# Kernel tuning notes

Measured on AMD Instinct MI355X. Metric: run time of the kernel, lower is better.

The kernel has to match this reference:

```python
import jax, jax.numpy as jnp
import numpy as np

BS, SEQ, ENC, DEC, HEADS, INTERM = 32, 2048, 512, 512, 8, 128
IH = INTERM * HEADS


def setup_inputs() -> dict:
    key = jax.random.key(0)
    ks = jax.random.split(key, 16)
    s = 0.02
    return {
        "enc": jax.random.normal(ks[0], (BS, SEQ, ENC), jnp.float32),
        "dec": jax.random.normal(ks[1], (BS, 1, DEC + ENC), jnp.float32),
        "kappa": jax.random.uniform(ks[2], (BS, 1, HEADS), jnp.float32),
        "mask": jnp.ones((BS, SEQ, 1), jnp.float32),
        "Wv": jax.random.normal(ks[3], (ENC, IH), jnp.float32) * s,
        "bv": jnp.zeros((IH,), jnp.float32),
        "Wq": jax.random.normal(ks[4], (DEC + ENC, IH), jnp.float32) * s,
        "bq": jnp.zeros((IH,), jnp.float32),
        "Wf": jax.random.normal(ks[5], (IH, HEADS), jnp.float32) * s,
        "bf": jnp.zeros((HEADS,), jnp.float32),
        "Wb": jax.random.normal(ks[6], (DEC + ENC, HEADS), jnp.float32) * s,
        "bb": jnp.zeros((HEADS,), jnp.float32),
        "Wk": jax.random.normal(ks[7], (DEC + ENC, HEADS), jnp.float32) * s,
        "bk": jnp.zeros((HEADS,), jnp.float32),
        "Wfc": jax.random.normal(ks[8], (ENC * HEADS, ENC), jnp.float32) * s,
        "bfc": jnp.zeros((ENC,), jnp.float32),
    }


def reference(enc, dec, kappa, mask, Wv, bv, Wq, bq, Wf, bf, Wb, bb, Wk, bk, Wfc, bfc):
    bs, seq_len, _ = enc.shape
    sp = jax.nn.softplus
    value = enc @ Wv + bv                      # (bs, seq, IH)
    query = dec @ Wq + bq                      # (bs, 1, IH), broadcasts over seq
    alpha = sp(jnp.tanh(query + value) @ Wf + bf) * mask   # (bs, seq, heads)
    beta = sp(dec @ Wb + bb)                   # (bs, 1, heads)
    kappa = kappa + sp(dec @ Wk + bk)          # (bs, 1, heads)
    u = jnp.arange(seq_len, dtype=enc.dtype)[None, :, None]
    score = alpha * jnp.exp(-beta * (kappa - u) ** 2)       # (bs, seq, heads)
    # weighted reduction over seq: (bs, heads, enc) then flatten in heads-major order
    context = jnp.einsum("bsh,bse->bhe", score, enc).reshape(bs, -1)
    context = context @ Wfc + bfc              # (bs, enc)
    return context[:, None, :], kappa, score
```

## Files before the change

### kernel.cpp

```cpp
#include <hip/hip_runtime.h>
#include <cstdint>
#include <cstddef>

#define BSZ    32
#define SEQL   2048
#define ENCD   512
#define DE     1024
#define NHEADS 8
#define IHD    1024

typedef unsigned short u16;
typedef __bf16 bf16x8 __attribute__((ext_vector_type(8)));
typedef float floatx4 __attribute__((ext_vector_type(4)));
typedef unsigned short u16x8 __attribute__((ext_vector_type(8)));

__device__ __forceinline__ u16 f2bf(float f) {
    unsigned int u = __float_as_uint(f);
    u = (u + 0x7FFFu + ((u >> 16) & 1u)) >> 16;
    return (u16)u;
}
__device__ __forceinline__ float bf2f(u16 v) {
    return __uint_as_float(((unsigned int)v) << 16);
}
__device__ __forceinline__ float softplus_f(float x) {
    return fmaxf(x, 0.0f) + log1pf(__expf(-fabsf(x)));
}
__device__ __forceinline__ float tanh_fast(float x) {
    const float e = __expf(2.0f * x);
    return 1.0f - 2.0f / (e + 1.0f);
}
__device__ __forceinline__ void async_cp16(u16* lds, const u16* g) {
    __builtin_amdgcn_global_load_lds(
        (const __attribute__((address_space(1))) unsigned int*)g,
        (__attribute__((address_space(3))) unsigned int*)lds, 16, 0, 0);
}

__global__ __launch_bounds__(256) void pre_kernel(
    const float* __restrict__ enc, u16* __restrict__ enc_bf,
    const float* __restrict__ Wv, const float* __restrict__ Wf,
    u16* __restrict__ WvT, u16* __restrict__ wfb,
    const float* __restrict__ dec, const float* __restrict__ kappa_in,
    const float* __restrict__ Wq, const float* __restrict__ bq,
    const float* __restrict__ bv,
    const float* __restrict__ Wb, const float* __restrict__ bb,
    const float* __restrict__ Wk, const float* __restrict__ bk,
    float* __restrict__ query_ws, float* __restrict__ beta_ws,
    float* __restrict__ kappa_out)
{
    __shared__ float sh[64 * 65];
    const int bid = blockIdx.x, tid = threadIdx.x;

    if (bid < 16384) {
        const size_t i = (size_t)bid * 256 + tid;
        const float4* p = (const float4*)enc + i * 2;
        const float4 a = p[0], b2 = p[1];
        u16x8 o;
        o[0] = f2bf(a.x);  o[1] = f2bf(a.y);  o[2] = f2bf(a.z);  o[3] = f2bf(a.w);
        o[4] = f2bf(b2.x); o[5] = f2bf(b2.y); o[6] = f2bf(b2.z); o[7] = f2bf(b2.w);
        *((u16x8*)enc_bf + i) = o;
        return;
    }
    if (bid < 16512) {
        const int tb = bid - 16384;
        const int nt = tb & 15, kt = tb >> 4;
        for (int i = tid; i < 4096; i += 256) {
            const int kk = i >> 6, nn = i & 63;
            sh[kk * 65 + nn] = Wv[(size_t)(kt * 64 + kk) * IHD + nt * 64 + nn];
        }
        __syncthreads();
        for (int i = tid; i < 4096; i += 256) {
            const int nn = i >> 6, kk = i & 63;
            WvT[(size_t)(nt * 64 + nn) * 512 + kt * 64 + kk] = f2bf(sh[kk * 65 + nn]);
        }
        return;
    }
    if (bid == 16512) {
        for (int i = tid; i < 8192; i += 256) {
            const int j   = i & 7;
            const int fr8 = (i >> 3) & 7;
            const int qd  = (i >> 6) & 3;
            const int ks  = (i >> 8) & 3;
            const int nn  = i >> 10;
            const int row = nn * 128 + ks * 32 + qd * 8 + j;
            wfb[i] = f2bf(Wf[row * NHEADS + fr8]);
        }
        return;
    }
    const int p = bid - 16513;
    const int b = p & 31, y = p >> 5;
    float* s_dec = sh;
    float* s_red = sh + DE;
    for (int i = tid; i < DE; i += 256) s_dec[i] = dec[b * DE + i];
    __syncthreads();

    if (y < 32) {
        const int cl = tid & 31, kg = tid >> 5;
        const int col = y * 32 + cl;
        float a = 0.f;
        const float* w = Wq + col;
        #pragma unroll 4
        for (int k = kg * 128; k < kg * 128 + 128; ++k)
            a = fmaf(s_dec[k], w[(size_t)k * IHD], a);
        s_red[tid] = a;
        __syncthreads();
        if (tid < 32) {
            float s = 0.f;
            #pragma unroll
            for (int i = 0; i < 8; ++i) s += s_red[i * 32 + tid];
            query_ws[(size_t)b * IHD + col] = s + bq[col] + bv[col];
        }
    } else {
        const int h = tid & 7, kg = tid >> 3;
        float ab = 0.f, ak = 0.f;
        for (int k = kg * 32; k < kg * 32 + 32; ++k) {
            const float d = s_dec[k];
            ab = fmaf(d, Wb[k * NHEADS + h], ab);
            ak = fmaf(d, Wk[k * NHEADS + h], ak);
        }
        s_red[tid] = ab;
        __syncthreads();
        for (int off = 128; off >= 8; off >>= 1) {
            if (tid < off) s_red[tid] += s_red[tid + off];
            __syncthreads();
        }
        const float abT = (tid < 8) ? s_red[tid] : 0.f;
        __syncthreads();
        s_red[tid] = ak;
        __syncthreads();
        for (int off = 128; off >= 8; off >>= 1) {
            if (tid < off) s_red[tid] += s_red[tid + off];
            __syncthreads();
        }
        if (tid < 8) {
            beta_ws[b * NHEADS + tid]   = softplus_f(bb[tid] + abT);
            kappa_out[b * NHEADS + tid] = kappa_in[b * NHEADS + tid]
                                        + softplus_f(bk[tid] + s_red[tid]);
        }
    }
}

#define BM 128

__global__ __launch_bounds__(256, 2) void gemm_score_ctx_kernel(
    const u16* __restrict__ encb, const u16* __restrict__ wvT,
    const u16* __restrict__ wfb2, const float* __restrict__ bf_g,
    const float* __restrict__ mask, const float* __restrict__ query_ws,
    const float* __restrict__ beta_ws, const float* __restrict__ kappa_out,
    float* __restrict__ score_out, float* __restrict__ ctx_part)
{
    __shared__ __align__(16) unsigned char smem[69632];
    u16*   tT      = (u16*)(smem + 32768);
    float* s_score = (float*)(smem + 65536);

    const int tid  = threadIdx.x;
    const int m0   = blockIdx.x * BM;
    const int b    = blockIdx.x >> 4;
    const int sc   = blockIdx.x & 15;
    const int lane = tid & 63;
    const int w    = tid >> 6;
    const int wr   = w >> 1, wc = w & 1;
    const int fr   = lane & 15, quad = lane >> 4;

    int mA[4], csA[4];
    #pragma unroll
    for (int r = 0; r < 4; ++r) {
        const int c = r * 256 + tid;
        mA[r]  = c >> 3;
        csA[r] = (c & 7) ^ (mA[r] & 7);
    }

    auto stage = [&](int bufsel, int it) {
        u16* Ab = (u16*)(smem + bufsel * 32768);
        u16* Bb = Ab + 8192;
        const int nn2 = it >> 3, kt2 = it & 7;
        const size_t aoff = (size_t)kt2 * 64;
        const size_t boff = (size_t)nn2 * (128 * 512) + (size_t)kt2 * 64;
        #pragma unroll
        for (int r = 0; r < 4; ++r) {
            async_cp16(Ab + (r * 256 + (tid & 192)) * 8,
                       encb + (size_t)(m0 + mA[r]) * 512 + aoff + csA[r] * 8);
            async_cp16(Bb + (size_t)(r * 256 + (tid & 192)) * 8,
                       wvT + (size_t)mA[r] * 512 + boff + csA[r] * 8);
        }
    };

    floatx4 acc2[2] = {};

    stage(0, 0);

    for (int nn = 0; nn < 8; ++nn) {
        const int n0 = nn * 128;
        float qv[4];
        bf16x8 wfr[4];
        floatx4 acc[4][4] = {};

        #pragma unroll
        for (int kt = 0; kt < 8; ++kt) {
            const int it = nn * 8 + kt;
            if (kt < 7 || nn < 7)
                stage((it + 1) & 1, it + 1);
            if (kt == 0) {
                #pragma unroll
                for (int nt = 0; nt < 4; ++nt)
                    qv[nt] = query_ws[(size_t)b * IHD + n0 + wc * 64 + nt * 16 + fr];
                #pragma unroll
                for (int ks = 0; ks < 4; ++ks)
                    wfr[ks] = *(const bf16x8*)&wfb2[((nn * 4 + ks) * 4 + quad) * 64
                                                    + (fr & 7) * 8];
            }
            if (kt == 7 && nn == 7) {
                asm volatile("s_waitcnt vmcnt(0)" ::: "memory");
            } else if (kt == 0) {
                asm volatile("s_waitcnt vmcnt(16)" ::: "memory");
            } else {
                asm volatile("s_waitcnt vmcnt(8)" ::: "memory");
            }
            __builtin_amdgcn_sched_barrier(0);
            __builtin_amdgcn_s_barrier();

            u16* Ab = (u16*)(smem + (it & 1) * 32768);
            u16* Bb = Ab + 8192;
            __builtin_amdgcn_s_setprio(1);
            #pragma unroll
            for (int s2 = 0; s2 < 2; ++s2) {
                bf16x8 af[4], bfr[4];
                #pragma unroll
                for (int mt = 0; mt < 4; ++mt) {
                    const int ma = wr * 64 + mt * 16 + fr;
                    const int ca = (s2 * 4 + quad) ^ (ma & 7);
                    af[mt] = *(const bf16x8*)&Ab[ma * 64 + ca * 8];
                }
                #pragma unroll
                for (int nt = 0; nt < 4; ++nt) {
                    const int nb = wc * 64 + nt * 16 + fr;
                    const int cb = (s2 * 4 + quad) ^ (nb & 7);
                    bfr[nt] = *(const bf16x8*)&Bb[nb * 64 + cb * 8];
                }
                #pragma unroll
                for (int mt = 0; mt < 4; ++mt)
                    #pragma unroll
                    for (int nt = 0; nt < 4; ++nt)
                        acc[mt][nt] = __builtin_amdgcn_mfma_f32_16x16x32_bf16(
                            af[mt], bfr[nt], acc[mt][nt], 0, 0, 0);
            }
            __builtin_amdgcn_s_setprio(0);
            __builtin_amdgcn_sched_barrier(0);
            __builtin_amdgcn_s_barrier();
        }

        #pragma unroll
        for (int mt = 0; mt < 4; ++mt) {
            #pragma unroll
            for (int nt = 0; nt < 4; ++nt) {
                const int col = wc * 64 + nt * 16 + fr;
                #pragma unroll
                for (int reg = 0; reg < 4; ++reg) {
                    const int row = wr * 64 + mt * 16 + quad * 4 + reg;
                    ((__bf16*)tT)[row * 128 + (col ^ ((row & 7) << 3))] =
                        (__bf16)tanh_fast(acc[mt][nt][reg] + qv[nt]);
                }
            }
        }
        asm volatile("s_waitcnt lgkmcnt(0)" ::: "memory");
        __builtin_amdgcn_sched_barrier(0);
        __builtin_amdgcn_s_barrier();

        #pragma unroll
        for (int t = 0; t < 2; ++t) {
            const int row = w * 32 + t * 16 + fr;
            #pragma unroll
            for (int ks = 0; ks < 4; ++ks) {
                const bf16x8 ta = *(const bf16x8*)
                    &tT[row * 128 + ((ks * 32 + quad * 8) ^ ((row & 7) << 3))];
                acc2[t] = __builtin_amdgcn_mfma_f32_16x16x32_bf16(ta, wfr[ks], acc2[t], 0, 0, 0);
            }
        }
        __builtin_amdgcn_sched_barrier(0);
        __builtin_amdgcn_s_barrier();
    }

    if (fr < NHEADS) {
        const float bfh = bf_g[fr];
        const float bet = beta_ws[b * NHEADS + fr];
        const float kap = kappa_out[b * NHEADS + fr];
        #pragma unroll
        for (int t = 0; t < 2; ++t) {
            #pragma unroll
            for (int reg = 0; reg < 4; ++reg) {
                const int row  = w * 32 + t * 16 + quad * 4 + reg;
                const int grow = m0 + row;
                const int s = grow & 2047;
                const float alpha = softplus_f(acc2[t][reg] + bfh) * mask[grow];
                const float du = kap - (float)s;
                const float v = alpha * __expf(-bet * du * du);
                score_out[(size_t)grow * NHEADS + fr] = v;
                s_score[row * NHEADS + fr] = v;
            }
        }
    }
    asm volatile("s_waitcnt lgkmcnt(0)" ::: "memory");
    __builtin_amdgcn_s_barrier();

    {
        float acc0[8] = {}, acc1[8] = {};
        const u16* ep = encb + (size_t)m0 * 512 + lane * 8;
        #pragma unroll 4
        for (int s = 0; s < 128; ++s) {
            const u16x8 ev = *(const u16x8*)(ep + (size_t)s * 512);
            const float2 sc2 = *(const float2*)&s_score[s * NHEADS + 2 * w];
            #pragma unroll
            for (int j = 0; j < 8; ++j) {
                const float e = bf2f(ev[j]);
                acc0[j] = fmaf(sc2.x, e, acc0[j]);
                acc1[j] = fmaf(sc2.y, e, acc1[j]);
            }
        }
        const int e8 = lane * 8;
        float* outp = ctx_part + ((size_t)sc * BSZ + b) * (NHEADS * ENCD);
        *(float4*)&outp[(2 * w + 0) * ENCD + e8]     = make_float4(acc0[0], acc0[1], acc0[2], acc0[3]);
        *(float4*)&outp[(2 * w + 0) * ENCD + e8 + 4] = make_float4(acc0[4], acc0[5], acc0[6], acc0[7]);
        *(float4*)&outp[(2 * w + 1) * ENCD + e8]     = make_float4(acc1[0], acc1[1], acc1[2], acc1[3]);
        *(float4*)&outp[(2 * w + 1) * ENCD + e8 + 4] = make_float4(acc1[4], acc1[5], acc1[6], acc1[7]);
    }
}

__global__ __launch_bounds__(256) void ctx_reduce_kernel(
    const float* __restrict__ part, float* __restrict__ ctx_ws)
{
    const int i = blockIdx.x * 256 + threadIdx.x;
    float a = 0.f;
    #pragma unroll
    for (int sc = 0; sc < 16; ++sc)
        a += part[(size_t)sc * 131072 + i];
    ctx_ws[i] = a;
}

__global__ __launch_bounds__(256) void final_kernel(
    const float* __restrict__ ctx_ws, const float* __restrict__ Wfc,
    const float* __restrict__ bfc, float* __restrict__ out_ctx)
{
    __shared__ float s_ctx[32][128];
    const int jc = blockIdx.x, ks = blockIdx.y, tid = threadIdx.x;
    const int jl = tid & 31, bg = tid >> 5;
    const int j = jc * 32 + jl;
    float a0 = 0.f, a1 = 0.f, a2 = 0.f, a3 = 0.f;

    for (int t = 0; t < 4; ++t) {
        const int k0 = ks * 512 + t * 128;
        __syncthreads();
        for (int i = tid; i < 32 * 128; i += 256) {
            const int bb2 = i >> 7, kk = i & 127;
            s_ctx[bb2][kk] = ctx_ws[(size_t)bb2 * (NHEADS * ENCD) + k0 + kk];
        }
        __syncthreads();
        for (int kk = 0; kk < 128; ++kk) {
            const float wv = Wfc[(size_t)(k0 + kk) * ENCD + j];
            a0 = fmaf(s_ctx[bg * 4 + 0][kk], wv, a0);
            a1 = fmaf(s_ctx[bg * 4 + 1][kk], wv, a1);
            a2 = fmaf(s_ctx[bg * 4 + 2][kk], wv, a2);
            a3 = fmaf(s_ctx[bg * 4 + 3][kk], wv, a3);
        }
    }
    const float bias = (ks == 0) ? bfc[j] : 0.0f;
    atomicAdd(&out_ctx[(bg * 4 + 0) * ENCD + j], a0 + bias);
    atomicAdd(&out_ctx[(bg * 4 + 1) * ENCD + j], a1 + bias);
    atomicAdd(&out_ctx[(bg * 4 + 2) * ENCD + j], a2 + bias);
    atomicAdd(&out_ctx[(bg * 4 + 3) * ENCD + j], a3 + bias);
}

extern "C" void kernel_launch(void* const* d_in, const int* in_sizes, int n_in,
                              void* d_out, int out_size, void* d_ws, size_t ws_size,
                              hipStream_t stream)
{
    const float* enc   = (const float*)d_in[0];
    const float* dec   = (const float*)d_in[1];
    const float* kapin = (const float*)d_in[2];
    const float* mask  = (const float*)d_in[3];
    const float* Wv    = (const float*)d_in[4];
    const float* bv    = (const float*)d_in[5];
    const float* Wq    = (const float*)d_in[6];
    const float* bq    = (const float*)d_in[7];
    const float* Wf    = (const float*)d_in[8];
    const float* bf    = (const float*)d_in[9];
    const float* Wb    = (const float*)d_in[10];
    const float* bb    = (const float*)d_in[11];
    const float* Wk    = (const float*)d_in[12];
    const float* bk    = (const float*)d_in[13];
    const float* Wfc   = (const float*)d_in[14];
    const float* bfc   = (const float*)d_in[15];

    float* out       = (float*)d_out;
    float* out_ctx   = out;
    float* out_kappa = out + 16384;
    float* out_score = out + 16640;

    char* w = (char*)d_ws;
    u16*   enc_bf   = (u16*)w;
    float* ctx_part = (float*)(w + 67108864);
    u16*   wvT      = (u16*)(w + 75497472);
    float* q_ws     = (float*)(w + 76546048);
    float* beta_ws  = (float*)(w + 76677120);
    float* ctx_ws   = (float*)(w + 76678144);
    u16*   wfb      = (u16*)(w + 77202432);

    hipMemsetAsync(out_ctx, 0, 16384 * sizeof(float), stream);

    pre_kernel<<<dim3(16384 + 128 + 1 + 1056), dim3(256), 0, stream>>>(
        enc, enc_bf, Wv, Wf, wvT, wfb,
        dec, kapin, Wq, bq, bv, Wb, bb, Wk, bk, q_ws, beta_ws, out_kappa);

    gemm_score_ctx_kernel<<<dim3((BSZ * SEQL) / BM), dim3(256), 0, stream>>>(
        enc_bf, wvT, wfb, bf, mask, q_ws, beta_ws, out_kappa,
        out_score, ctx_part);

    ctx_reduce_kernel<<<dim3(512), dim3(256), 0, stream>>>(ctx_part, ctx_ws);

    final_kernel<<<dim3(16, 8), dim3(256), 0, stream>>>(
        ctx_ws, Wfc, bfc, out_ctx);
}
```

Before: 420.0 us.

## Fuse enc bf16 conversion into GEMM kernel prologue and widen final_kernel grid

Moves the fp32-to-bf16 conversion of enc out of pre_kernel and into the start of the fused GEMM/score kernel. Each block converts its own 128-row tile and writes it to the workspace before the main loop. The main loop reads that tile back with async LDS loads, so the block waits on vmcnt and a barrier first. This removes the large conversion grid from pre_kernel but puts the write-then-read round trip on the critical path of every GEMM block, and it relies on global-write visibility within the block. The final_kernel grid grows from 8 to 32 K-splits so each block handles one 128-chunk, which adds parallelism at the cost of more atomics.

After: 398.1 us. 5.2% less time.

```diff
diff --git a/kernel.cpp b/kernel.cpp
--- a/kernel.cpp
+++ b/kernel.cpp
@@ -36,7 +36,6 @@
 }
 
 __global__ __launch_bounds__(256) void pre_kernel(
-    const float* __restrict__ enc, u16* __restrict__ enc_bf,
     const float* __restrict__ Wv, const float* __restrict__ Wf,
     u16* __restrict__ WvT, u16* __restrict__ wfb,
     const float* __restrict__ dec, const float* __restrict__ kappa_in,
@@ -50,19 +49,8 @@
     __shared__ float sh[64 * 65];
     const int bid = blockIdx.x, tid = threadIdx.x;
 
-    if (bid < 16384) {
-        const size_t i = (size_t)bid * 256 + tid;
-        const float4* p = (const float4*)enc + i * 2;
-        const float4 a = p[0], b2 = p[1];
-        u16x8 o;
-        o[0] = f2bf(a.x);  o[1] = f2bf(a.y);  o[2] = f2bf(a.z);  o[3] = f2bf(a.w);
-        o[4] = f2bf(b2.x); o[5] = f2bf(b2.y); o[6] = f2bf(b2.z); o[7] = f2bf(b2.w);
-        *((u16x8*)enc_bf + i) = o;
-        return;
-    }
-    if (bid < 16512) {
-        const int tb = bid - 16384;
-        const int nt = tb & 15, kt = tb >> 4;
+    if (bid < 128) {
+        const int nt = bid & 15, kt = bid >> 4;
         for (int i = tid; i < 4096; i += 256) {
             const int kk = i >> 6, nn = i & 63;
             sh[kk * 65 + nn] = Wv[(size_t)(kt * 64 + kk) * IHD + nt * 64 + nn];
@@ -74,7 +62,7 @@
         }
         return;
     }
-    if (bid == 16512) {
+    if (bid == 128) {
         for (int i = tid; i < 8192; i += 256) {
             const int j   = i & 7;
             const int fr8 = (i >> 3) & 7;
@@ -86,7 +74,7 @@
         }
         return;
     }
-    const int p = bid - 16513;
+    const int p = bid - 129;
     const int b = p & 31, y = p >> 5;
     float* s_dec = sh;
     float* s_red = sh + DE;
@@ -142,7 +130,8 @@
 #define BM 128
 
 __global__ __launch_bounds__(256, 2) void gemm_score_ctx_kernel(
-    const u16* __restrict__ encb, const u16* __restrict__ wvT,
+    const float* __restrict__ enc, u16* __restrict__ encb,
+    const u16* __restrict__ wvT,
     const u16* __restrict__ wfb2, const float* __restrict__ bf_g,
     const float* __restrict__ mask, const float* __restrict__ query_ws,
     const float* __restrict__ beta_ws, const float* __restrict__ kappa_out,
@@ -160,6 +149,21 @@
     const int w    = tid >> 6;
     const int wr   = w >> 1, wc = w & 1;
     const int fr   = lane & 15, quad = lane >> 4;
+
+    {
+        const float4* src = (const float4*)enc + (size_t)m0 * 128;
+        u16x8* dst = (u16x8*)(encb + (size_t)m0 * 512);
+        for (int i = tid; i < 8192; i += 256) {
+            const float4 a = src[i * 2], b2 = src[i * 2 + 1];
+            u16x8 o;
+            o[0] = f2bf(a.x);  o[1] = f2bf(a.y);  o[2] = f2bf(a.z);  o[3] = f2bf(a.w);
+            o[4] = f2bf(b2.x); o[5] = f2bf(b2.y); o[6] = f2bf(b2.z); o[7] = f2bf(b2.w);
+            dst[i] = o;
+        }
+        asm volatile("s_waitcnt vmcnt(0)" ::: "memory");
+        __builtin_amdgcn_sched_barrier(0);
+        __builtin_amdgcn_s_barrier();
+    }
 
     int mA[4], csA[4];
     #pragma unroll
@@ -343,23 +347,21 @@
     const int jc = blockIdx.x, ks = blockIdx.y, tid = threadIdx.x;
     const int jl = tid & 31, bg = tid >> 5;
     const int j = jc * 32 + jl;
+    const int k0 = ks * 128;
+
+    for (int i = tid; i < 32 * 128; i += 256) {
+        const int bb2 = i >> 7, kk = i & 127;
+        s_ctx[bb2][kk] = ctx_ws[(size_t)bb2 * (NHEADS * ENCD) + k0 + kk];
+    }
+    __syncthreads();
+
     float a0 = 0.f, a1 = 0.f, a2 = 0.f, a3 = 0.f;
-
-    for (int t = 0; t < 4; ++t) {
-        const int k0 = ks * 512 + t * 128;
-        __syncthreads();
-        for (int i = tid; i < 32 * 128; i += 256) {
-            const int bb2 = i >> 7, kk = i & 127;
-            s_ctx[bb2][kk] = ctx_ws[(size_t)bb2 * (NHEADS * ENCD) + k0 + kk];
-        }
-        __syncthreads();
-        for (int kk = 0; kk < 128; ++kk) {
-            const float wv = Wfc[(size_t)(k0 + kk) * ENCD + j];
-            a0 = fmaf(s_ctx[bg * 4 + 0][kk], wv, a0);
-            a1 = fmaf(s_ctx[bg * 4 + 1][kk], wv, a1);
-            a2 = fmaf(s_ctx[bg * 4 + 2][kk], wv, a2);
-            a3 = fmaf(s_ctx[bg * 4 + 3][kk], wv, a3);
-        }
+    for (int kk = 0; kk < 128; ++kk) {
+        const float wv = Wfc[(size_t)(k0 + kk) * ENCD + j];
+        a0 = fmaf(s_ctx[bg * 4 + 0][kk], wv, a0);
+        a1 = fmaf(s_ctx[bg * 4 + 1][kk], wv, a1);
+        a2 = fmaf(s_ctx[bg * 4 + 2][kk], wv, a2);
+        a3 = fmaf(s_ctx[bg * 4 + 3][kk], wv, a3);
     }
     const float bias = (ks == 0) ? bfc[j] : 0.0f;
     atomicAdd(&out_ctx[(bg * 4 + 0) * ENCD + j], a0 + bias);
@@ -405,16 +407,16 @@
 
     hipMemsetAsync(out_ctx, 0, 16384 * sizeof(float), stream);
 
-    pre_kernel<<<dim3(16384 + 128 + 1 + 1056), dim3(256), 0, stream>>>(
-        enc, enc_bf, Wv, Wf, wvT, wfb,
+    pre_kernel<<<dim3(128 + 1 + 1056), dim3(256), 0, stream>>>(
+        Wv, Wf, wvT, wfb,
         dec, kapin, Wq, bq, bv, Wb, bb, Wk, bk, q_ws, beta_ws, out_kappa);
 
     gemm_score_ctx_kernel<<<dim3((BSZ * SEQL) / BM), dim3(256), 0, stream>>>(
-        enc_bf, wvT, wfb, bf, mask, q_ws, beta_ws, out_kappa,
+        enc, enc_bf, wvT, wfb, bf, mask, q_ws, beta_ws, out_kappa,
         out_score, ctx_part);
 
     ctx_reduce_kernel<<<dim3(512), dim3(256), 0, stream>>>(ctx_part, ctx_ws);
 
-    final_kernel<<<dim3(16, 8), dim3(256), 0, stream>>>(
+    final_kernel<<<dim3(16, 32), dim3(256), 0, stream>>>(
         ctx_ws, Wfc, bfc, out_ctx);
 }
```
